# Performance work log

Measured on AMD Instinct MI355X. Metric: run time of the kernel, lower is better.

Reference implementation:

```python
import jax, jax.numpy as jnp
import numpy as np

EMBED_DIM = 1024
ATTEN_DIM = 64


def setup_inputs() -> dict:
    key = jax.random.key(0)
    k_x, k_q, k_k, k_v = jax.random.split(key, 4)
    B, S = 4, 4096
    scale = 1.0 / np.sqrt(EMBED_DIM)
    x = jax.random.normal(k_x, (B, S, EMBED_DIM), dtype=jnp.float32)
    # torch nn.Linear weights are [out_features, in_features]
    Wq = jax.random.normal(k_q, (ATTEN_DIM, EMBED_DIM), dtype=jnp.float32) * scale
    Wk = jax.random.normal(k_k, (ATTEN_DIM, EMBED_DIM), dtype=jnp.float32) * scale
    Wv = jax.random.normal(k_v, (ATTEN_DIM, EMBED_DIM), dtype=jnp.float32) * scale
    return {"x": x, "Wq": Wq, "Wk": Wk, "Wv": Wv}


def reference(x, Wq, Wk, Wv):
    # q, k, v: [B, S, D]
    q = jnp.einsum('bse,de->bsd', x, Wq)
    k = jnp.einsum('bse,de->bsd', x, Wk)
    v = jnp.einsum('bse,de->bsd', x, Wv)
    d = k.shape[-1]
    scores = jnp.einsum('bsd,btd->bst', q, k) / jnp.sqrt(jnp.float32(d))
    S = x.shape[1]
    causal = jnp.tril(jnp.ones((S, S), dtype=bool))
    scores = jnp.where(causal[None, :, :], scores, -jnp.inf)
    attn = jax.nn.softmax(scores, axis=-1)
    return jnp.einsum('bst,btd->bsd', attn, v)
```

## Files before the change

### kernel.cpp

```cpp
#include <hip/hip_runtime.h>
#include <hip/hip_bf16.h>
#include <stdint.h>

typedef __attribute__((ext_vector_type(8))) short  short8;
typedef __attribute__((ext_vector_type(4))) short  short4v;
typedef __attribute__((ext_vector_type(4))) float  float4v;
typedef __attribute__((ext_vector_type(16))) float f32x16;
typedef __attribute__((ext_vector_type(2))) unsigned int uint2v;

#define MFMA16(a, b, c) __builtin_amdgcn_mfma_f32_16x16x32_bf16((a), (b), (c), 0, 0, 0)
#define MFMA32(a, b, c) __builtin_amdgcn_mfma_f32_32x32x16_bf16((a), (b), (c), 0, 0, 0)

#define S_LEN  4096
#define NBATCH 4
#define EMB    1024
#define DD     64
#define NROWS  (NBATCH * S_LEN)
#define SCL2   0.1803368801111204f

#define AS1 const __attribute__((address_space(1))) unsigned int*
#define AS3 __attribute__((address_space(3))) unsigned int*

static __device__ __forceinline__ short f2bf(float f) {
  uint32_t u = __float_as_uint(f);
  return (short)((u + 0x7FFFu + ((u >> 16) & 1u)) >> 16);
}
static __device__ __forceinline__ unsigned pk2(float a, float b) {
  union { __hip_bfloat162 h; unsigned u; } z;
  z.h = __float22bfloat162_rn(make_float2(a, b));
  return z.u;
}
static __device__ __forceinline__ short8 cvt8(float4v a, float4v b) {
  union { unsigned u[4]; short8 s; } z;
  z.u[0] = pk2(a[0], a[1]); z.u[1] = pk2(a[2], a[3]);
  z.u[2] = pk2(b[0], b[1]); z.u[3] = pk2(b[2], b[3]);
  return z.s;
}

__global__ void wcvt_kernel(const float* __restrict__ Wq, const float* __restrict__ Wk,
                            const float* __restrict__ Wv, short* __restrict__ Wb2) {
  const int t   = blockIdx.x * 256 + threadIdx.x;
  const int row = t >> 7;
  const int k   = (t & 127) * 8;
  const float* src = (row < 64) ? (Wq + (size_t)row * EMB)
                   : (row < 128) ? (Wk + (size_t)(row - 64) * EMB)
                                 : (Wv + (size_t)(row - 128) * EMB);
  const float sc = (row < 64) ? SCL2 : 1.0f;
  float4v a = *(const float4v*)(src + k);
  float4v b = *(const float4v*)(src + k + 4);
#pragma unroll
  for (int i = 0; i < 4; ++i) { a[i] *= sc; b[i] *= sc; }
  *(short8*)(Wb2 + (((k >> 5) * 192 + row) << 5) + (k & 31)) = cvt8(a, b);
}

__global__ __launch_bounds__(256, 2) void qkv_kernel(
    const float* __restrict__ x, const short* __restrict__ Wb2,
    short* __restrict__ Qb, short* __restrict__ Kb, short* __restrict__ Vt) {
  __shared__ float As[2][2048];
  __shared__ short Bs[2][12288];

  const int tid  = threadIdx.x;
  const int w    = tid >> 6;
  const int lane = tid & 63;
  const int ln   = lane & 15;
  const int quad = lane >> 4;
  const int m0   = blockIdx.x * 32;
  const int wr   = w & 1;
  const int wc   = w >> 1;

  const int tA0 = 2 * w, tA1 = 2 * w + 1;
  const float* xA0 = x + (size_t)(m0 + ((tA0 >> 2) << 4) + (lane >> 2)) * EMB
                       + ((tA0 & 3) * 4 + (lane & 3)) * 4;
  const float* xA1 = x + (size_t)(m0 + ((tA1 >> 2) << 4) + (lane >> 2)) * EMB
                       + ((tA1 & 3) * 4 + (lane & 3)) * 4;
  const short* wB = Wb2 + (size_t)(6 * w) * 512 + lane * 8;

#define STAGE(S, BUF) do {                                                      \
    __builtin_amdgcn_global_load_lds((AS1)(xA0 + (S) * 64),                     \
        (AS3)&As[BUF][tA0 * 256], 16, 0, 0);                                    \
    __builtin_amdgcn_global_load_lds((AS1)(xA1 + (S) * 64),                     \
        (AS3)&As[BUF][tA1 * 256], 16, 0, 0);                                    \
    _Pragma("unroll")                                                           \
    for (int j = 0; j < 6; ++j)                                                 \
      __builtin_amdgcn_global_load_lds((AS1)(wB + (size_t)(S) * 12288 + j * 512),\
          (AS3)&Bs[BUF][(6 * w + j) * 512], 16, 0, 0);                          \
  } while (0)

  const float4v zz = {0.f, 0.f, 0.f, 0.f};
  float4v acc[6] = {zz, zz, zz, zz, zz, zz};

  STAGE(0, 0);
  int buf = 0;
  for (int s = 0; s < 16; ++s) {
    __syncthreads();
    if (s + 1 < 16) STAGE(s + 1, buf ^ 1);
    short8 aF[2];
#pragma unroll
    for (int h = 0; h < 2; ++h) {
      const int ai = (wr * 4 + 2 * h + (quad >> 1)) * 256 + (ln * 4 + (quad & 1) * 2) * 4;
      const float4v lo = *(const float4v*)&As[buf][ai];
      const float4v hi = *(const float4v*)&As[buf][ai + 4];
      aF[h] = cvt8(lo, hi);
    }
#pragma unroll
    for (int f = 0; f < 6; ++f) {
      const int cf = wc * 6 + f;
      const short8 b0 = *(const short8*)&Bs[buf][(cf * 16 + ln) * 32 + quad * 8];
      const short8 b1 = *(const short8*)&Bs[buf][6144 + (cf * 16 + ln) * 32 + quad * 8];
      if (wc == 0 || f < 2) {
        acc[f] = MFMA16(aF[0], b0, acc[f]);
        acc[f] = MFMA16(aF[1], b1, acc[f]);
      } else {
        acc[f] = MFMA16(b0, aF[0], acc[f]);
        acc[f] = MFMA16(b1, aF[1], acc[f]);
      }
    }
    buf ^= 1;
  }
#undef STAGE

  const int b  = m0 >> 12;
  const int sb = m0 & (S_LEN - 1);
  if (wc == 0) {
#pragma unroll
    for (int f = 0; f < 6; ++f)
#pragma unroll
      for (int r = 0; r < 4; ++r) {
        const int row = m0 + wr * 16 + quad * 4 + r;
        if (f < 4) Qb[(size_t)row * DD + f * 16 + ln] = f2bf(acc[f][r]);
        else       Kb[(size_t)row * DD + (f - 4) * 16 + ln] = f2bf(acc[f][r]);
      }
  } else {
#pragma unroll
    for (int f = 0; f < 2; ++f)
#pragma unroll
      for (int r = 0; r < 4; ++r) {
        const int row = m0 + wr * 16 + quad * 4 + r;
        Kb[(size_t)row * DD + 32 + f * 16 + ln] = f2bf(acc[f][r]);
      }
#pragma unroll
    for (int f = 2; f < 6; ++f)
#pragma unroll
      for (int r = 0; r < 4; ++r) {
        const int d = (f - 2) * 16 + quad * 4 + r;
        Vt[((size_t)b * DD + d) * S_LEN + sb + wr * 16 + ln] = f2bf(acc[f][r]);
      }
  }
}

__global__ __launch_bounds__(512, 2) void attn_kernel(
    const short* __restrict__ Qb, const short* __restrict__ Kb,
    const short* __restrict__ Vt, float* __restrict__ out) {
  __shared__ float sbuf[8][2048];
  __shared__ float llds[8][32];

  const int tid  = threadIdx.x;
  const int w    = tid >> 6;
  const int lane = tid & 63;
  const int l31  = lane & 31;
  const int hi   = lane >> 5;
  const int g    = blockIdx.x;
  const int u    = g & 255;
  const int half = g >> 8;
  const int b    = u & 3;
  const int jj   = u >> 2;
  const int band = half ? (127 - jj) : jj;
  const short* Kbase = Kb + (size_t)b * S_LEN * DD;
  const short* Vbase = Vt + (size_t)b * DD * S_LEN;

  const int qb    = band * 32;
  const int qg0   = b * S_LEN + qb;
  const int qglob = qb + l31;

  short8 q8[4];
#pragma unroll
  for (int dk = 0; dk < 4; ++dk)
    q8[dk] = *(const short8*)(Qb + (size_t)(qg0 + l31) * DD + dk * 16 + hi * 8);

  f32x16 o0, o1;
  f32x16 zz16;
#pragma unroll
  for (int e = 0; e < 16; ++e) { o0[e] = 0.f; o1[e] = 0.f; zz16[e] = 0.f; }
  float lp = 0.f;

  const int T = (qb + 95) >> 6;

  for (int it = w; it < T; it += 8) {
    const int kv0 = it * 64;
    short8 kf[2][4];
#pragma unroll
    for (int c = 0; c < 2; ++c)
#pragma unroll
      for (int dk = 0; dk < 4; ++dk)
        kf[c][dk] = *(const short8*)(Kbase + (size_t)(kv0 + c * 32 + l31) * DD + dk * 16 + hi * 8);
    short8 vf[2][4];
#pragma unroll
    for (int df = 0; df < 2; ++df)
#pragma unroll
      for (int kc = 0; kc < 4; ++kc)
        vf[df][kc] = *(const short8*)(Vbase + (size_t)(df * 32 + l31) * S_LEN + kv0 + kc * 16 + hi * 8);

    f32x16 s0 = MFMA32(kf[0][0], q8[0], zz16);
    f32x16 s1 = MFMA32(kf[1][0], q8[0], zz16);
#pragma unroll
    for (int dk = 1; dk < 4; ++dk) {
      s0 = MFMA32(kf[0][dk], q8[dk], s0);
      s1 = MFMA32(kf[1][dk], q8[dk], s1);
    }

    if (kv0 + 63 > qb) {
#pragma unroll
      for (int e = 0; e < 16; ++e) {
        const int kvl = (e & 3) + 8 * (e >> 2) + 4 * hi;
        float e0 = __builtin_amdgcn_exp2f(fminf(s0[e], 60.0f));
        if (kv0 + kvl > qglob) e0 = 0.f;
        float e1 = __builtin_amdgcn_exp2f(fminf(s1[e], 60.0f));
        if (kv0 + 32 + kvl > qglob) e1 = 0.f;
        s0[e] = e0; s1[e] = e1;
        lp += e0 + e1;
      }
    } else {
#pragma unroll
      for (int e = 0; e < 16; ++e) {
        float e0 = __builtin_amdgcn_exp2f(fminf(s0[e], 60.0f));
        float e1 = __builtin_amdgcn_exp2f(fminf(s1[e], 60.0f));
        s0[e] = e0; s1[e] = e1;
        lp += e0 + e1;
      }
    }

#define PACK_PV(S, V00, V01, V10, V11) do {                                     \
    unsigned ua, ub, uc, ud, ue, uf2, ug, uh;                                   \
    asm("v_cvt_pk_bf16_f32 %0, %1, %2" : "=v"(ua) : "v"((S)[0]),  "v"((S)[1])); \
    asm("v_cvt_pk_bf16_f32 %0, %1, %2" : "=v"(ub) : "v"((S)[2]),  "v"((S)[3])); \
    asm("v_cvt_pk_bf16_f32 %0, %1, %2" : "=v"(uc) : "v"((S)[4]),  "v"((S)[5])); \
    asm("v_cvt_pk_bf16_f32 %0, %1, %2" : "=v"(ud) : "v"((S)[6]),  "v"((S)[7])); \
    asm("v_cvt_pk_bf16_f32 %0, %1, %2" : "=v"(ue) : "v"((S)[8]),  "v"((S)[9])); \
    asm("v_cvt_pk_bf16_f32 %0, %1, %2" : "=v"(uf2): "v"((S)[10]), "v"((S)[11]));\
    asm("v_cvt_pk_bf16_f32 %0, %1, %2" : "=v"(ug) : "v"((S)[12]), "v"((S)[13]));\
    asm("v_cvt_pk_bf16_f32 %0, %1, %2" : "=v"(uh) : "v"((S)[14]), "v"((S)[15]));\
    uint2v r0 = __builtin_amdgcn_permlane32_swap(ua, uc, false, false);         \
    uint2v r1 = __builtin_amdgcn_permlane32_swap(ub, ud, false, false);         \
    uint2v r2 = __builtin_amdgcn_permlane32_swap(ue, ug, false, false);         \
    uint2v r3 = __builtin_amdgcn_permlane32_swap(uf2, uh, false, false);        \
    union { unsigned uu[4]; short8 s8; } p0, p1;                                \
    p0.uu[0] = r0[0]; p0.uu[1] = r1[0]; p0.uu[2] = r0[1]; p0.uu[3] = r1[1];     \
    p1.uu[0] = r2[0]; p1.uu[1] = r3[0]; p1.uu[2] = r2[1]; p1.uu[3] = r3[1];     \
    o0 = MFMA32(p0.s8, (V00), o0);                                              \
    o0 = MFMA32(p1.s8, (V01), o0);                                              \
    o1 = MFMA32(p0.s8, (V10), o1);                                              \
    o1 = MFMA32(p1.s8, (V11), o1);                                              \
  } while (0)

    PACK_PV(s0, vf[0][0], vf[0][1], vf[1][0], vf[1][1]);
    PACK_PV(s1, vf[0][2], vf[0][3], vf[1][2], vf[1][3]);
#undef PACK_PV
  }

  lp += __shfl_xor(lp, 32);
  float* pw = &sbuf[w][0];
#pragma unroll
  for (int e = 0; e < 16; ++e) {
    const int ql = (e & 3) + 8 * (e >> 2) + 4 * hi;
    pw[ql * 64 + l31]      = o0[e];
    pw[ql * 64 + 32 + l31] = o1[e];
  }
  if (hi == 0) llds[w][l31] = lp;
  __syncthreads();

#pragma unroll
  for (int jx = 0; jx < 4; ++jx) {
    const int idx = tid + jx * 512;
    const int row = idx >> 6, col = idx & 63;
    float sum = 0.f, lt = 0.f;
#pragma unroll
    for (int wi = 0; wi < 8; ++wi) {
      sum += sbuf[wi][row * 64 + col];
      lt  += llds[wi][row];
    }
    out[(size_t)(qg0 + row) * DD + col] = sum * __builtin_amdgcn_rcpf(lt);
  }
}

extern "C" void kernel_launch(void* const* d_in, const int* in_sizes, int n_in,
                              void* d_out, int out_size, void* d_ws, size_t ws_size,
                              hipStream_t stream) {
  const float* x  = (const float*)d_in[0];
  const float* Wq = (const float*)d_in[1];
  const float* Wk = (const float*)d_in[2];
  const float* Wv = (const float*)d_in[3];

  short* Qb  = (short*)d_ws;
  short* Kb  = Qb + (size_t)NROWS * DD;
  short* Vt  = Kb + (size_t)NROWS * DD;
  short* Wb2 = Vt + (size_t)NROWS * DD;

  wcvt_kernel<<<dim3(96), dim3(256), 0, stream>>>(Wq, Wk, Wv, Wb2);
  qkv_kernel<<<dim3(NROWS / 32), dim3(256), 0, stream>>>(x, Wb2, Qb, Kb, Vt);
  attn_kernel<<<dim3(NBATCH * 128), dim3(512), 0, stream>>>(Qb, Kb, Vt, (float*)d_out);
}
```

Measured before the change: 155.4 us.

## Shrink attention KV step to 32 keys and raise occupancy hint to four blocks

The attention inner loop now handles 32 keys per iteration instead of 64, so only the diagonal tile needs masking and the trip count per query band is band+1. The smaller per-iteration register footprint lets launch_bounds request four blocks per CU instead of two. This cuts wasted masked work on the diagonal and aims to hide latency through occupancy. In exchange each iteration does half the MFMA work per load batch, which means more loop overhead and less instruction-level parallelism, and LDS use (about 65KB per block for sbuf) may cap real occupancy regardless of the hint.

```diff
diff --git a/kernel.cpp b/kernel.cpp
--- a/kernel.cpp
+++ b/kernel.cpp
@@ -148,7 +148,7 @@
   }
 }
 
-__global__ __launch_bounds__(512, 2) void attn_kernel(
+__global__ __launch_bounds__(512, 4) void attn_kernel(
     const short* __restrict__ Qb, const short* __restrict__ Kb,
     const short* __restrict__ Vt, float* __restrict__ out) {
   __shared__ float sbuf[8][2048];
@@ -183,78 +183,66 @@
   for (int e = 0; e < 16; ++e) { o0[e] = 0.f; o1[e] = 0.f; zz16[e] = 0.f; }
   float lp = 0.f;
 
-  const int T = (qb + 95) >> 6;
-
-  for (int it = w; it < T; it += 8) {
-    const int kv0 = it * 64;
-    short8 kf[2][4];
-#pragma unroll
-    for (int c = 0; c < 2; ++c)
-#pragma unroll
-      for (int dk = 0; dk < 4; ++dk)
-        kf[c][dk] = *(const short8*)(Kbase + (size_t)(kv0 + c * 32 + l31) * DD + dk * 16 + hi * 8);
-    short8 vf[2][4];
+  const int T32 = band + 1;
+
+  for (int it = w; it < T32; it += 8) {
+    const int kv0 = it * 32;
+    short8 kf[4];
+#pragma unroll
+    for (int dk = 0; dk < 4; ++dk)
+      kf[dk] = *(const short8*)(Kbase + (size_t)(kv0 + l31) * DD + dk * 16 + hi * 8);
+    short8 vf[2][2];
 #pragma unroll
     for (int df = 0; df < 2; ++df)
 #pragma unroll
-      for (int kc = 0; kc < 4; ++kc)
+      for (int kc = 0; kc < 2; ++kc)
         vf[df][kc] = *(const short8*)(Vbase + (size_t)(df * 32 + l31) * S_LEN + kv0 + kc * 16 + hi * 8);
 
-    f32x16 s0 = MFMA32(kf[0][0], q8[0], zz16);
-    f32x16 s1 = MFMA32(kf[1][0], q8[0], zz16);
-#pragma unroll
-    for (int dk = 1; dk < 4; ++dk) {
-      s0 = MFMA32(kf[0][dk], q8[dk], s0);
-      s1 = MFMA32(kf[1][dk], q8[dk], s1);
-    }
-
-    if (kv0 + 63 > qb) {
+    f32x16 s = MFMA32(kf[0], q8[0], zz16);
+#pragma unroll
+    for (int dk = 1; dk < 4; ++dk)
+      s = MFMA32(kf[dk], q8[dk], s);
+
+    if (it == band) {
 #pragma unroll
       for (int e = 0; e < 16; ++e) {
         const int kvl = (e & 3) + 8 * (e >> 2) + 4 * hi;
-        float e0 = __builtin_amdgcn_exp2f(fminf(s0[e], 60.0f));
+        float e0 = __builtin_amdgcn_exp2f(fminf(s[e], 60.0f));
         if (kv0 + kvl > qglob) e0 = 0.f;
-        float e1 = __builtin_amdgcn_exp2f(fminf(s1[e], 60.0f));
-        if (kv0 + 32 + kvl > qglob) e1 = 0.f;
-        s0[e] = e0; s1[e] = e1;
-        lp += e0 + e1;
+        s[e] = e0;
+        lp += e0;
       }
     } else {
 #pragma unroll
       for (int e = 0; e < 16; ++e) {
-        float e0 = __builtin_amdgcn_exp2f(fminf(s0[e], 60.0f));
-        float e1 = __builtin_amdgcn_exp2f(fminf(s1[e], 60.0f));
-        s0[e] = e0; s1[e] = e1;
-        lp += e0 + e1;
-      }
-    }
-
-#define PACK_PV(S, V00, V01, V10, V11) do {                                     \
-    unsigned ua, ub, uc, ud, ue, uf2, ug, uh;                                   \
-    asm("v_cvt_pk_bf16_f32 %0, %1, %2" : "=v"(ua) : "v"((S)[0]),  "v"((S)[1])); \
-    asm("v_cvt_pk_bf16_f32 %0, %1, %2" : "=v"(ub) : "v"((S)[2]),  "v"((S)[3])); \
-    asm("v_cvt_pk_bf16_f32 %0, %1, %2" : "=v"(uc) : "v"((S)[4]),  "v"((S)[5])); \
-    asm("v_cvt_pk_bf16_f32 %0, %1, %2" : "=v"(ud) : "v"((S)[6]),  "v"((S)[7])); \
-    asm("v_cvt_pk_bf16_f32 %0, %1, %2" : "=v"(ue) : "v"((S)[8]),  "v"((S)[9])); \
-    asm("v_cvt_pk_bf16_f32 %0, %1, %2" : "=v"(uf2): "v"((S)[10]), "v"((S)[11]));\
-    asm("v_cvt_pk_bf16_f32 %0, %1, %2" : "=v"(ug) : "v"((S)[12]), "v"((S)[13]));\
-    asm("v_cvt_pk_bf16_f32 %0, %1, %2" : "=v"(uh) : "v"((S)[14]), "v"((S)[15]));\
-    uint2v r0 = __builtin_amdgcn_permlane32_swap(ua, uc, false, false);         \
-    uint2v r1 = __builtin_amdgcn_permlane32_swap(ub, ud, false, false);         \
-    uint2v r2 = __builtin_amdgcn_permlane32_swap(ue, ug, false, false);         \
-    uint2v r3 = __builtin_amdgcn_permlane32_swap(uf2, uh, false, false);        \
-    union { unsigned uu[4]; short8 s8; } p0, p1;                                \
-    p0.uu[0] = r0[0]; p0.uu[1] = r1[0]; p0.uu[2] = r0[1]; p0.uu[3] = r1[1];     \
-    p1.uu[0] = r2[0]; p1.uu[1] = r3[0]; p1.uu[2] = r2[1]; p1.uu[3] = r3[1];     \
-    o0 = MFMA32(p0.s8, (V00), o0);                                              \
-    o0 = MFMA32(p1.s8, (V01), o0);                                              \
-    o1 = MFMA32(p0.s8, (V10), o1);                                              \
-    o1 = MFMA32(p1.s8, (V11), o1);                                              \
-  } while (0)
-
-    PACK_PV(s0, vf[0][0], vf[0][1], vf[1][0], vf[1][1]);
-    PACK_PV(s1, vf[0][2], vf[0][3], vf[1][2], vf[1][3]);
-#undef PACK_PV
+        float e0 = __builtin_amdgcn_exp2f(fminf(s[e], 60.0f));
+        s[e] = e0;
+        lp += e0;
+      }
+    }
+
+    {
+      unsigned ua, ub, uc, ud, ue, uf2, ug, uh;
+      asm("v_cvt_pk_bf16_f32 %0, %1, %2" : "=v"(ua) : "v"(s[0]),  "v"(s[1]));
+      asm("v_cvt_pk_bf16_f32 %0, %1, %2" : "=v"(ub) : "v"(s[2]),  "v"(s[3]));
+      asm("v_cvt_pk_bf16_f32 %0, %1, %2" : "=v"(uc) : "v"(s[4]),  "v"(s[5]));
+      asm("v_cvt_pk_bf16_f32 %0, %1, %2" : "=v"(ud) : "v"(s[6]),  "v"(s[7]));
+      asm("v_cvt_pk_bf16_f32 %0, %1, %2" : "=v"(ue) : "v"(s[8]),  "v"(s[9]));
+      asm("v_cvt_pk_bf16_f32 %0, %1, %2" : "=v"(uf2): "v"(s[10]), "v"(s[11]));
+      asm("v_cvt_pk_bf16_f32 %0, %1, %2" : "=v"(ug) : "v"(s[12]), "v"(s[13]));
+      asm("v_cvt_pk_bf16_f32 %0, %1, %2" : "=v"(uh) : "v"(s[14]), "v"(s[15]));
+      uint2v r0 = __builtin_amdgcn_permlane32_swap(ua, uc, false, false);
+      uint2v r1 = __builtin_amdgcn_permlane32_swap(ub, ud, false, false);
+      uint2v r2 = __builtin_amdgcn_permlane32_swap(ue, ug, false, false);
+      uint2v r3 = __builtin_amdgcn_permlane32_swap(uf2, uh, false, false);
+      union { unsigned uu[4]; short8 s8; } p0, p1;
+      p0.uu[0] = r0[0]; p0.uu[1] = r1[0]; p0.uu[2] = r0[1]; p0.uu[3] = r1[1];
+      p1.uu[0] = r2[0]; p1.uu[1] = r3[0]; p1.uu[2] = r2[1]; p1.uu[3] = r3[1];
+      o0 = MFMA32(p0.s8, vf[0][0], o0);
+      o0 = MFMA32(p1.s8, vf[0][1], o0);
+      o1 = MFMA32(p0.s8, vf[1][0], o1);
+      o1 = MFMA32(p1.s8, vf[1][1], o1);
+    }
   }
 
   lp += __shfl_xor(lp, 32);
```

New measurement: 153.9 us. Within noise of the previous version (-1.0%).
